# Kernel tuning notes

Hardware: AMD Instinct MI355X
Metric: run time of the kernel (lower is better)

## Reference

```python
import jax, jax.numpy as jnp
import numpy as np

NUM_HEADS = 16
CHUNK = 128


def _bitlinear(x, w, b):
    # BitLinear 1.58b: ternary weights + int8 activations with STE (forward value is exact quantized math)
    w_scale = jnp.maximum(jnp.mean(jnp.abs(w)), 1e-5)
    w_norm = w / w_scale
    w_q = jax.lax.stop_gradient(jnp.sign(w_norm) - w_norm) + w_norm
    x_scale = jnp.maximum(jnp.max(jnp.abs(x), axis=-1, keepdims=True), 1e-5)
    x_norm = x / x_scale * 127.0
    x_q = jax.lax.stop_gradient(jnp.round(x_norm) - x_norm) + x_norm
    return jnp.einsum('...i,oi->...o', x_q, w_q) * (x_scale * w_scale / 127.0) + b


def _rmsnorm(x, w, eps=1e-6):
    return x * jax.lax.rsqrt(jnp.mean(x * x, axis=-1, keepdims=True) + eps) * w


def setup_inputs():
    key = jax.random.key(0)
    ks = jax.random.split(key, 8)
    B, N, C = 2, 4096, 2048
    def w(k, shape):
        return jax.random.normal(k, shape, jnp.float32) * 0.02
    return {
        'x': jax.random.normal(ks[0], (B, N, C), jnp.float32),
        'qkv_w': w(ks[1], (3 * C, C)), 'qkv_b': w(ks[2], (3 * C,)),
        'gate_w': w(ks[3], (C, C)), 'gate_b': w(ks[4], (C,)),
        'proj_w': w(ks[5], (C, C)), 'proj_b': w(ks[6], (C,)),
        'norm_w': jnp.ones((C,), jnp.float32),
    }


def reference(x, qkv_w, qkv_b, gate_w, gate_b, proj_w, proj_b, norm_w):
    B, N, C = x.shape
    H, L = NUM_HEADS, CHUNK
    D = C // H
    scale = D ** -0.5
    qkv = _bitlinear(x, qkv_w, qkv_b).reshape(B, N, 3, H, D)
    q, k, v = qkv[:, :, 0], qkv[:, :, 1], qkv[:, :, 2]
    g = jax.nn.sigmoid(_bitlinear(x, gate_w, gate_b)).reshape(B, N, H, D)
    nc = N // L  # N chosen as multiple of chunk_size -> pad branch is a no-op

    def chunks(t):  # (B,N,H,D) -> (nc,B,L,H,D) for scan over chunks
        return t.reshape(B, nc, L, H, D).transpose(1, 0, 2, 3, 4)
    qc, kc, vc, gc = map(chunks, (q, k, v, g))

    def step(kv_state, inp):
        qi, ki, vi, gi = inp  # each (B,L,H,D)
        # faithful to torch: qi @ ki.transpose(-2,-1) contracts head_dim per position -> (B,L,H,H)
        attn = jax.nn.softmax(jnp.einsum('blhd,blgd->blhg', qi, ki) * scale, axis=-1)
        local = jnp.einsum('blhg,blgd->blhd', attn, vi)
        recur = jnp.einsum('blhd,bhde->blhe', qi, kv_state)
        decay = jnp.mean(gi, axis=1)[..., None]          # (B,H,D,1)
        kv_update = jnp.einsum('blhd,blhe->bhde', ki, vi)
        return kv_state * decay + kv_update, local + recur

    kv0 = jnp.zeros((B, H, D, D), x.dtype)
    _, out = jax.lax.scan(step, kv0, (qc, kc, vc, gc))  # out: (nc,B,L,H,D)
    out = out.transpose(1, 0, 2, 3, 4).reshape(B, N, C)
    return _bitlinear(_rmsnorm(out, norm_w), proj_w, proj_b)
```

## Files before the change

kernel.cpp:

```cpp
#include <hip/hip_runtime.h>
#include <stdint.h>

typedef __attribute__((ext_vector_type(4))) float f32x4;
typedef __attribute__((ext_vector_type(8))) __bf16 bf16x8;
typedef __attribute__((ext_vector_type(4))) unsigned int u32x4;
typedef __attribute__((ext_vector_type(4))) int i32x4;

#define DEV static __device__ __forceinline__

DEV float bf2f(unsigned short h){ union{unsigned int u; float f;} v; v.u=((unsigned int)h)<<16; return v.f; }
DEV unsigned short f2bf(float f){ union{float ff; unsigned int u;} v; v.ff=f; unsigned int u=v.u;
  u += 0x7fffu + ((u>>16)&1u); return (unsigned short)(u>>16); }

DEV f32x4 mfma16(bf16x8 a, bf16x8 b, f32x4 c){
  return __builtin_amdgcn_mfma_f32_16x16x32_bf16(a, b, c, 0, 0, 0);
}
DEV i32x4 mfma_i8(i32x4 a, i32x4 b, i32x4 c){
  return __builtin_amdgcn_mfma_i32_16x16x64_i8(a, b, c, 0, 0, 0);
}

#define GLOAD_LDS16(gptr, ldsptr) \
  __builtin_amdgcn_global_load_lds( \
      (const __attribute__((address_space(1))) unsigned int*)(gptr), \
      (__attribute__((address_space(3))) unsigned int*)(ldsptr), 16, 0, 0)

__global__ __launch_bounds__(256) void k_quant_w(
    const float* __restrict__ wq, const float* __restrict__ wg, const float* __restrict__ wp,
    signed char* __restrict__ oq, signed char* __restrict__ og, signed char* __restrict__ op,
    float* __restrict__ partials)
{
  int blk = blockIdx.x, t = threadIdx.x;
  const float* src; signed char* dst; long base;
  if (blk < 3072){ src=wq; dst=oq; base=(long)blk*4096; }
  else if (blk < 4096){ src=wg; dst=og; base=(long)(blk-3072)*4096; }
  else { src=wp; dst=op; base=(long)(blk-4096)*4096; }
  float s = 0.f;
  #pragma unroll
  for (int i=0;i<4;i++){
    long e = base + (long)(i*256 + t)*4;
    float4 v = *reinterpret_cast<const float4*>(src + e);
    s += fabsf(v.x)+fabsf(v.y)+fabsf(v.z)+fabsf(v.w);
    signed char tmp[4];
    tmp[0] = (v.x>0.f)?1:((v.x<0.f)?-1:0);
    tmp[1] = (v.y>0.f)?1:((v.y<0.f)?-1:0);
    tmp[2] = (v.z>0.f)?1:((v.z<0.f)?-1:0);
    tmp[3] = (v.w>0.f)?1:((v.w<0.f)?-1:0);
    *reinterpret_cast<unsigned int*>(dst + e) = *reinterpret_cast<unsigned int*>(tmp);
  }
  #pragma unroll
  for (int m=1;m<64;m<<=1) s += __shfl_xor(s, m);
  __shared__ float red[4];
  if ((t&63)==0) red[t>>6]=s;
  __syncthreads();
  if (t==0) partials[blk] = red[0]+red[1]+red[2]+red[3];
}

__global__ void k_finalize(const float* __restrict__ partials, float* __restrict__ scales)
{
  int t = threadIdx.x;
  __shared__ float red[4];
  for (int w=0; w<3; w++){
    int s0 = (w==0)?0:((w==1)?3072:4096);
    int s1 = (w==0)?3072:((w==1)?4096:5120);
    float acc = 0.f;
    for (int i=s0+t; i<s1; i+=256) acc += partials[i];
    #pragma unroll
    for (int m=1;m<64;m<<=1) acc += __shfl_xor(acc, m);
    if ((t&63)==0) red[t>>6]=acc;
    __syncthreads();
    if (t==0){
      float total = red[0]+red[1]+red[2]+red[3];
      float denom = (w==0)? 12582912.0f : 4194304.0f;
      float wsc = fmaxf(total/denom, 1e-5f);
      scales[w] = wsc / 127.0f;
    }
    __syncthreads();
  }
}

__global__ __launch_bounds__(256) void k_quant_x(const float* __restrict__ x,
    signed char* __restrict__ xq, float* __restrict__ xs)
{
  int row=blockIdx.x, t=threadIdx.x;
  const float* xr = x + (long)row*2048;
  float v[8];
  float4 a = *reinterpret_cast<const float4*>(xr + t*8);
  float4 b = *reinterpret_cast<const float4*>(xr + t*8 + 4);
  v[0]=a.x; v[1]=a.y; v[2]=a.z; v[3]=a.w; v[4]=b.x; v[5]=b.y; v[6]=b.z; v[7]=b.w;
  float mx=0.f;
  #pragma unroll
  for (int j=0;j<8;j++) mx = fmaxf(mx, fabsf(v[j]));
  #pragma unroll
  for (int m=1;m<64;m<<=1) mx = fmaxf(mx, __shfl_xor(mx, m));
  __shared__ float red[4];
  if ((t&63)==0) red[t>>6]=mx;
  __syncthreads();
  float sc = fmaxf(fmaxf(fmaxf(red[0],red[1]),fmaxf(red[2],red[3])), 1e-5f);
  if (t==0) xs[row]=sc;
  signed char q[8];
  #pragma unroll
  for (int j=0;j<8;j++) q[j] = (signed char)(int)rintf((v[j]/sc)*127.f);
  *reinterpret_cast<uint2*>(xq + (long)row*2048 + t*8) = *reinterpret_cast<uint2*>(q);
}

template<int MODE>
__global__ __launch_bounds__(256) void k_gemm(
    const signed char* __restrict__ A, const signed char* __restrict__ Bw,
    const float* __restrict__ xs, const float* __restrict__ scales, const float* __restrict__ bias,
    unsigned short* __restrict__ oq, unsigned short* __restrict__ ok, unsigned short* __restrict__ ov,
    float* __restrict__ decay, float* __restrict__ of32)
{
  __shared__ signed char As[2][128*128];
  __shared__ signed char Bs[2][128*128];
  const int K = 2048, NT = 16;
  int tid=threadIdx.x;
  int bn=blockIdx.x, bm=blockIdx.y;
  long n0=(long)bn*128, m0=(long)bm*128;
  int wave=tid>>6, lane=tid&63, l15=lane&15, l4=lane>>4;
  int wr=wave>>1, wc=wave&1;
  int srow = wave*8 + (lane>>3);
  int scol = ((lane&7) ^ ((lane>>3)&7))*16;
  i32x4 z4 = {0,0,0,0};
  i32x4 acc[4][4];
  #pragma unroll
  for (int i=0;i<4;i++)
    #pragma unroll
    for (int j=0;j<4;j++) acc[i][j]=z4;

#define STAGE_ALL(buf, kt) do{ \
    GLOAD_LDS16(A  + (m0 +  0 + srow)*K + (kt) + scol, &As[buf][(  0 + wave*8)*128]); \
    GLOAD_LDS16(A  + (m0 + 32 + srow)*K + (kt) + scol, &As[buf][( 32 + wave*8)*128]); \
    GLOAD_LDS16(A  + (m0 + 64 + srow)*K + (kt) + scol, &As[buf][( 64 + wave*8)*128]); \
    GLOAD_LDS16(A  + (m0 + 96 + srow)*K + (kt) + scol, &As[buf][( 96 + wave*8)*128]); \
    GLOAD_LDS16(Bw + (n0 +  0 + srow)*K + (kt) + scol, &Bs[buf][(  0 + wave*8)*128]); \
    GLOAD_LDS16(Bw + (n0 + 32 + srow)*K + (kt) + scol, &Bs[buf][( 32 + wave*8)*128]); \
    GLOAD_LDS16(Bw + (n0 + 64 + srow)*K + (kt) + scol, &Bs[buf][( 64 + wave*8)*128]); \
    GLOAD_LDS16(Bw + (n0 + 96 + srow)*K + (kt) + scol, &Bs[buf][( 96 + wave*8)*128]); }while(0)
#define RD_A(buf, mr, kk) (*reinterpret_cast<const i32x4*>(&As[buf][(wr*64+(mr)*16+l15)*128 + ((((kk)*4+l4) ^ (l15&7))<<4)]))
#define RD_B(buf, nr, kk) (*reinterpret_cast<const i32x4*>(&Bs[buf][(wc*64+(nr)*16+l15)*128 + ((((kk)*4+l4) ^ (l15&7))<<4)]))

  STAGE_ALL(0, 0);

  for (int t=0; t<NT; ++t){
    int c = t&1;
    if (t+1 < NT){
      STAGE_ALL(c^1, (t+1)*128);
      asm volatile("s_waitcnt vmcnt(8)" ::: "memory");
    } else {
      asm volatile("s_waitcnt vmcnt(0)" ::: "memory");
    }
    __builtin_amdgcn_s_barrier();
    __builtin_amdgcn_s_setprio(1);
    #pragma unroll
    for (int kk=0;kk<2;kk++){
      i32x4 af[4], bfr[4];
      #pragma unroll
      for (int mr=0;mr<4;mr++) af[mr] = RD_A(c,mr,kk);
      #pragma unroll
      for (int nr=0;nr<4;nr++) bfr[nr] = RD_B(c,nr,kk);
      #pragma unroll
      for (int mr=0;mr<4;mr++)
        #pragma unroll
        for (int nr=0;nr<4;nr++)
          acc[mr][nr] = mfma_i8(af[mr], bfr[nr], acc[mr][nr]);
    }
    __builtin_amdgcn_s_setprio(0);
    if (t+1 < NT) __builtin_amdgcn_s_barrier();
  }

  float fac = scales[MODE];
  float xsv[4][4];
  #pragma unroll
  for (int mr=0;mr<4;mr++)
    #pragma unroll
    for (int r2=0;r2<4;r2++)
      xsv[mr][r2] = xs[m0 + wr*64 + mr*16 + 4*l4 + r2] * fac;

  if (MODE==0){
    int sidx = (int)(n0 >> 11);
    unsigned short* dst = (sidx==0)?oq:((sidx==1)?ok:ov);
    int c0 = (int)(n0 & 2047);
    #pragma unroll
    for (int nr=0;nr<4;nr++){
      int c = c0 + wc*64 + nr*16 + l15;
      float bv = bias[n0 + wc*64 + nr*16 + l15];
      #pragma unroll
      for (int mr=0;mr<4;mr++)
        #pragma unroll
        for (int r2=0;r2<4;r2++){
          long grow = m0 + wr*64 + mr*16 + 4*l4 + r2;
          dst[grow*2048 + c] = f2bf((float)acc[mr][nr][r2]*xsv[mr][r2] + bv);
        }
    }
  } else if (MODE==1){
    float* red = reinterpret_cast<float*>(As);
    #pragma unroll
    for (int nr=0;nr<4;nr++){
      float bv = bias[n0 + wc*64 + nr*16 + l15];
      float ssum = 0.f;
      #pragma unroll
      for (int mr=0;mr<4;mr++)
        #pragma unroll
        for (int r2=0;r2<4;r2++){
          float val = (float)acc[mr][nr][r2]*xsv[mr][r2] + bv;
          ssum += 1.f/(1.f + expf(-val));
        }
      ssum += __shfl_xor(ssum, 16);
      ssum += __shfl_xor(ssum, 32);
      if (l4==0) red[wr*128 + wc*64 + nr*16 + l15] = ssum;
    }
    __syncthreads();
    if (tid < 128){
      float d = (red[tid] + red[128+tid]) * (1.0f/128.0f);
      decay[((long)bm*16 + bn)*128 + tid] = d;
    }
  } else {
    #pragma unroll
    for (int nr=0;nr<4;nr++){
      long c = n0 + wc*64 + nr*16 + l15;
      float bv = bias[c];
      #pragma unroll
      for (int mr=0;mr<4;mr++)
        #pragma unroll
        for (int r2=0;r2<4;r2++){
          long grow = m0 + wr*64 + mr*16 + 4*l4 + r2;
          of32[grow*2048 + c] = (float)acc[mr][nr][r2]*xsv[mr][r2] + bv;
        }
    }
  }
#undef STAGE_ALL
#undef RD_A
#undef RD_B
}

__global__ __launch_bounds__(256) void k_attnA(const unsigned short* __restrict__ qb,
    const unsigned short* __restrict__ kb, const unsigned short* __restrict__ vb,
    unsigned short* __restrict__ aof)
{
  __shared__ unsigned short at[4][16*32];
  __shared__ unsigned short vT[4][128*40];
  int tid=threadIdx.x, wave=tid>>6, lane=tid&63, l15=lane&15, l4=lane>>4;
  const float SCALE = 0.08838834764831845f;

  for (int i=lane;i<16*32;i+=64) at[wave][i]=0;
  for (int i=lane;i<128*40;i+=64) vT[wave][i]=0;

  long token = (long)blockIdx.x*4 + wave;
  long base = token*2048;

  bf16x8 qf[4], kf[4];
  #pragma unroll
  for (int kk=0;kk<4;kk++){
    qf[kk] = *reinterpret_cast<const bf16x8*>(qb + base + l15*128 + kk*32 + l4*8);
    kf[kk] = *reinterpret_cast<const bf16x8*>(kb + base + l15*128 + kk*32 + l4*8);
  }
  {
    int g = lane>>2, e0 = (lane&3)*32;
    #pragma unroll
    for (int j=0;j<4;j++){
      u32x4 vv = *reinterpret_cast<const u32x4*>(vb + base + g*128 + e0 + j*8);
      unsigned short tmp[8];
      *reinterpret_cast<u32x4*>(tmp) = vv;
      #pragma unroll
      for (int t2=0;t2<8;t2++) vT[wave][(e0+j*8+t2)*40 + g] = tmp[t2];
    }
  }

  f32x4 s = {0.f,0.f,0.f,0.f};
  #pragma unroll
  for (int kk=0;kk<4;kk++) s = mfma16(qf[kk], kf[kk], s);

  #pragma unroll
  for (int r2=0;r2<4;r2++){
    float v = s[r2];
    float m = v;
    m = fmaxf(m, __shfl_xor(m,1)); m = fmaxf(m, __shfl_xor(m,2));
    m = fmaxf(m, __shfl_xor(m,4)); m = fmaxf(m, __shfl_xor(m,8));
    float p = expf((v-m)*SCALE);
    float sum = p;
    sum += __shfl_xor(sum,1); sum += __shfl_xor(sum,2);
    sum += __shfl_xor(sum,4); sum += __shfl_xor(sum,8);
    at[wave][(4*l4+r2)*32 + l15] = f2bf(p/sum);
  }
  __syncthreads();

  bf16x8 pa = *reinterpret_cast<const bf16x8*>(&at[wave][l15*32 + l4*8]);
  #pragma unroll
  for (int eb=0;eb<8;eb++){
    bf16x8 vf = *reinterpret_cast<const bf16x8*>(&vT[wave][(eb*16+l15)*40 + l4*8]);
    f32x4 z4 = {0.f,0.f,0.f,0.f};
    f32x4 o = mfma16(pa, vf, z4);
    #pragma unroll
    for (int r2=0;r2<4;r2++)
      aof[base + (long)(4*l4+r2)*128 + eb*16 + l15] = f2bf(o[r2]);
  }
}

__global__ __launch_bounds__(256) void k_updB1(
    const unsigned short* __restrict__ kb, const unsigned short* __restrict__ vb,
    float* __restrict__ upds)
{
  __shared__ unsigned short kT[128*128];
  __shared__ unsigned short vT[128*128];
  int bid=blockIdx.x;
  int ch = bid&31, h=(bid>>5)&15, b=bid>>9;
  int tid=threadIdx.x, wave=tid>>6, lane=tid&63, l15=lane&15, l4=lane>>4;
  long base = ((long)b*4096 + (long)ch*128)*2048 + h*128;

  #pragma unroll
  for (int i=0;i<8;i++){
    int s = tid + i*256;
    int l = s>>4, sl = s&15;
    unsigned short tmp[8];
    u32x4 v1 = *reinterpret_cast<const u32x4*>(kb + base + (long)l*2048 + sl*8);
    *reinterpret_cast<u32x4*>(tmp) = v1;
    #pragma unroll
    for (int j=0;j<8;j++){
      int d = sl*8+j;
      kT[d*128 + (((l>>3)^(d&15))<<3) + (l&7)] = tmp[j];
    }
    u32x4 v2 = *reinterpret_cast<const u32x4*>(vb + base + (long)l*2048 + sl*8);
    *reinterpret_cast<u32x4*>(tmp) = v2;
    #pragma unroll
    for (int j=0;j<8;j++){
      int e = sl*8+j;
      vT[e*128 + (((l>>3)^(e&15))<<3) + (l&7)] = tmp[j];
    }
  }
  __syncthreads();

  f32x4 z4 = {0.f,0.f,0.f,0.f};
  f32x4 acc[2][8];
  #pragma unroll
  for (int er=0;er<2;er++)
    #pragma unroll
    for (int dc=0;dc<8;dc++) acc[er][dc]=z4;

  #pragma unroll
  for (int kk=0;kk<4;kk++){
    bf16x8 xf[2];
    #pragma unroll
    for (int er=0;er<2;er++){
      int e = wave*32 + er*16 + l15;
      xf[er] = *reinterpret_cast<const bf16x8*>(vT + e*128 + (((kk*4+l4)^(e&15))<<3));
    }
    #pragma unroll
    for (int dc=0;dc<8;dc++){
      int d = dc*16 + l15;
      bf16x8 kf = *reinterpret_cast<const bf16x8*>(kT + d*128 + (((kk*4+l4)^(d&15))<<3));
      #pragma unroll
      for (int er=0;er<2;er++)
        acc[er][dc] = mfma16(xf[er], kf, acc[er][dc]);
    }
  }

  float* dst = upds + (long)bid*16384;
  #pragma unroll
  for (int er=0;er<2;er++)
    #pragma unroll
    for (int dc=0;dc<8;dc++)
      #pragma unroll
      for (int r2=0;r2<4;r2++){
        int e = wave*32 + er*16 + 4*l4 + r2;
        int d = dc*16 + l15;
        dst[e*128 + d] = acc[er][dc][r2];
      }
}

__global__ __launch_bounds__(256) void k_scanB2(float* __restrict__ buf,
    const float* __restrict__ decay)
{
  int bid=blockIdx.x;
  int strip = bid&7, bh = bid>>3;
  int b = bh>>4, h = bh&15;
  int t = threadIdx.x;
  int f0 = t, f1 = t + 256;
  int e0 = strip*16 + (f0>>5), d0 = (f0&31)*4;
  int e1 = strip*16 + (f1>>5);
  long base = (long)bh * 32 * 16384;
  long o0 = (long)e0*128 + d0;
  long o1 = (long)e1*128 + d0;
  float4 s0 = {0.f,0.f,0.f,0.f}, s1 = {0.f,0.f,0.f,0.f};
  for (int ch=0; ch<32; ch++){
    float* p = buf + base + (long)ch*16384;
    float4 u0 = *reinterpret_cast<float4*>(p + o0);
    float4 u1 = *reinterpret_cast<float4*>(p + o1);
    *reinterpret_cast<float4*>(p + o0) = s0;
    *reinterpret_cast<float4*>(p + o1) = s1;
    float4 dc = *reinterpret_cast<const float4*>(decay + ((long)(b*32+ch)*16 + h)*128 + d0);
    s0.x = s0.x*dc.x + u0.x; s0.y = s0.y*dc.y + u0.y;
    s0.z = s0.z*dc.z + u0.z; s0.w = s0.w*dc.w + u0.w;
    s1.x = s1.x*dc.x + u1.x; s1.y = s1.y*dc.y + u1.y;
    s1.z = s1.z*dc.z + u1.z; s1.w = s1.w*dc.w + u1.w;
  }
}

__global__ __launch_bounds__(256) void k_recurB3(
    const unsigned short* __restrict__ qb, const float* __restrict__ upds,
    unsigned short* __restrict__ aof)
{
  __shared__ unsigned short sh[128*128];
  __shared__ unsigned short slo[128*128];
  int bid=blockIdx.x;
  int ch = bid&31, h=(bid>>5)&15, b=bid>>9;
  int tid=threadIdx.x, wave=tid>>6, lane=tid&63, l15=lane&15, l4=lane>>4;
  long slab = (long)bid*16384;
  long base = ((long)b*4096 + (long)ch*128)*2048 + h*128;

  #pragma unroll
  for (int i=0;i<8;i++){
    int s = tid + i*256;
    int e = s>>4, sl = s&15;
    float4 a = *reinterpret_cast<const float4*>(upds + slab + (long)e*128 + sl*8);
    float4 c = *reinterpret_cast<const float4*>(upds + slab + (long)e*128 + sl*8 + 4);
    float vv[8] = {a.x,a.y,a.z,a.w,c.x,c.y,c.z,c.w};
    unsigned short hi[8], lo[8];
    #pragma unroll
    for (int j=0;j<8;j++){
      hi[j] = f2bf(vv[j]);
      lo[j] = f2bf(vv[j] - bf2f(hi[j]));
    }
    int slot = e*128 + ((sl ^ (e&15))<<3);
    *reinterpret_cast<u32x4*>(sh + slot)  = *reinterpret_cast<u32x4*>(hi);
    *reinterpret_cast<u32x4*>(slo + slot) = *reinterpret_cast<u32x4*>(lo);
  }

  bf16x8 qf[2][4];
  #pragma unroll
  for (int mr=0;mr<2;mr++)
    #pragma unroll
    for (int kk=0;kk<4;kk++)
      qf[mr][kk] = *reinterpret_cast<const bf16x8*>(qb + base + (long)(wave*32+mr*16+l15)*2048 + kk*32 + l4*8);
  __syncthreads();

  f32x4 z4 = {0.f,0.f,0.f,0.f};
  f32x4 acc[2][8];
  #pragma unroll
  for (int mr=0;mr<2;mr++)
    #pragma unroll
    for (int ec=0;ec<8;ec++) acc[mr][ec]=z4;

  #pragma unroll
  for (int kk=0;kk<4;kk++)
    #pragma unroll
    for (int ec=0;ec<8;ec++){
      int e = ec*16 + l15;
      int slot = (((kk*4+l4)^(e&15))<<3);
      bf16x8 tfh = *reinterpret_cast<const bf16x8*>(sh + e*128 + slot);
      bf16x8 tfl = *reinterpret_cast<const bf16x8*>(slo + e*128 + slot);
      #pragma unroll
      for (int mr=0;mr<2;mr++){
        acc[mr][ec] = mfma16(qf[mr][kk], tfh, acc[mr][ec]);
        acc[mr][ec] = mfma16(qf[mr][kk], tfl, acc[mr][ec]);
      }
    }

  #pragma unroll
  for (int mr=0;mr<2;mr++)
    #pragma unroll
    for (int ec=0;ec<8;ec++)
      #pragma unroll
      for (int r2=0;r2<4;r2++){
        long o = base + (long)(wave*32+mr*16+4*l4+r2)*2048 + ec*16 + l15;
        aof[o] = f2bf(bf2f(aof[o]) + acc[mr][ec][r2]);
      }
}

__global__ __launch_bounds__(256) void k_rmsnorm_quant(const unsigned short* __restrict__ ain,
    const float* __restrict__ normw, signed char* __restrict__ x2q, float* __restrict__ xs2)
{
  int row=blockIdx.x, t=threadIdx.x;
  const unsigned short* rp = ain + (long)row*2048;
  u32x4 raw = *reinterpret_cast<const u32x4*>(rp + t*8);
  unsigned short tmp[8];
  *reinterpret_cast<u32x4*>(tmp) = raw;
  float xv[8]; float ss=0.f;
  #pragma unroll
  for (int j=0;j<8;j++){ xv[j]=bf2f(tmp[j]); ss += xv[j]*xv[j]; }
  #pragma unroll
  for (int m=1;m<64;m<<=1) ss += __shfl_xor(ss, m);
  __shared__ float red[4];
  if ((t&63)==0) red[t>>6]=ss;
  __syncthreads();
  float ms = (red[0]+red[1]+red[2]+red[3])*(1.0f/2048.0f) + 1e-6f;
  float rs = 1.0f/sqrtf(ms);
  __syncthreads();
  float4 w0 = *reinterpret_cast<const float4*>(normw + t*8);
  float4 w1 = *reinterpret_cast<const float4*>(normw + t*8 + 4);
  float wv[8] = {w0.x,w0.y,w0.z,w0.w,w1.x,w1.y,w1.z,w1.w};
  float y[8]; float mx=0.f;
  #pragma unroll
  for (int j=0;j<8;j++){ y[j] = xv[j]*rs*wv[j]; mx = fmaxf(mx, fabsf(y[j])); }
  #pragma unroll
  for (int m=1;m<64;m<<=1) mx = fmaxf(mx, __shfl_xor(mx, m));
  __shared__ float red2[4];
  if ((t&63)==0) red2[t>>6]=mx;
  __syncthreads();
  float sc = fmaxf(fmaxf(fmaxf(red2[0],red2[1]),fmaxf(red2[2],red2[3])), 1e-5f);
  if (t==0) xs2[row]=sc;
  signed char q[8];
  #pragma unroll
  for (int j=0;j<8;j++) q[j] = (signed char)(int)rintf((y[j]/sc)*127.f);
  *reinterpret_cast<uint2*>(x2q + (long)row*2048 + t*8) = *reinterpret_cast<uint2*>(q);
}

extern "C" void kernel_launch(void* const* d_in, const int* in_sizes, int n_in,
                              void* d_out, int out_size, void* d_ws, size_t ws_size,
                              hipStream_t stream)
{
  const float* x      = (const float*)d_in[0];
  const float* qkv_w  = (const float*)d_in[1];
  const float* qkv_b  = (const float*)d_in[2];
  const float* gate_w = (const float*)d_in[3];
  const float* gate_b = (const float*)d_in[4];
  const float* proj_w = (const float*)d_in[5];
  const float* proj_b = (const float*)d_in[6];
  const float* norm_w = (const float*)d_in[7];
  (void)in_sizes; (void)n_in; (void)out_size; (void)ws_size;

  char* ws = (char*)d_ws;
  const size_t MB = 1024UL*1024UL;
  signed char* wq_proj = (signed char*)(ws + 0*MB);
  signed char* wq_qkv  = (signed char*)(ws + 4*MB);
  signed char* wq_gate = (signed char*)(ws + 16*MB);
  signed char* xq      = (signed char*)(ws + 20*MB);
  float*       upds    = (float*)(ws + 4*MB);
  unsigned short* qb   = (unsigned short*)(ws + 68*MB);
  unsigned short* kb   = (unsigned short*)(ws + 100*MB);
  unsigned short* vb   = (unsigned short*)(ws + 132*MB);
  unsigned short* aof  = (unsigned short*)(ws + 164*MB);
  signed char* x2q     = (signed char*)qb;
  float* xs       = (float*)(ws + 196*MB);
  float* xs2      = xs + 8192;
  float* decay    = xs2 + 8192;
  float* partials = decay + 131072;
  float* scales   = partials + 5120;

  k_quant_w<<<5120,256,0,stream>>>(qkv_w, gate_w, proj_w, wq_qkv, wq_gate, wq_proj, partials);
  k_finalize<<<1,256,0,stream>>>(partials, scales);
  k_quant_x<<<8192,256,0,stream>>>(x, xq, xs);
  k_gemm<0><<<dim3(48,64),256,0,stream>>>(xq, wq_qkv, xs, scales, qkv_b,
      qb,kb,vb, nullptr, nullptr);
  k_gemm<1><<<dim3(16,64),256,0,stream>>>(xq, wq_gate, xs, scales, gate_b,
      nullptr,nullptr,nullptr, decay, nullptr);
  k_attnA<<<2048,256,0,stream>>>(qb,kb,vb, aof);
  k_updB1<<<1024,256,0,stream>>>(kb, vb, upds);
  k_scanB2<<<256,256,0,stream>>>(upds, decay);
  k_recurB3<<<1024,256,0,stream>>>(qb, upds, aof);
  k_rmsnorm_quant<<<8192,256,0,stream>>>(aof, norm_w, x2q, xs2);
  k_gemm<2><<<dim3(16,64),256,0,stream>>>(x2q, wq_proj, xs2, scales, proj_b,
      nullptr,nullptr,nullptr, nullptr, (float*)d_out);
}
```

Baseline: 402.5 us.

## Fuse QKV and gate GEMMs into one launch with XCD-aware tile swizzle

The QKV and gate projection GEMMs now run as a single launch over 64 column tiles. This relies on the gate weights sitting right after the QKV weights in the workspace. Blocks with bn>=48 run the gate/decay epilogue, and the rest write q/k/v. A new 1D block-to-tile mapping spreads consecutive block IDs across the 8 XCDs and groups tiles into 8x8 supertiles, so tiles sharing A and B operands run on the same L2. The aim is to improve cache reuse and cut launch and tail overhead. The cost is that correctness now depends on that workspace layout.

```diff
diff --git a/kernel.cpp b/kernel.cpp
--- a/kernel.cpp
+++ b/kernel.cpp
@@ -103,10 +103,11 @@
   *reinterpret_cast<uint2*>(xq + (long)row*2048 + t*8) = *reinterpret_cast<uint2*>(q);
 }
 
-template<int MODE>
+template<int MODE, int NBN>
 __global__ __launch_bounds__(256) void k_gemm(
     const signed char* __restrict__ A, const signed char* __restrict__ Bw,
-    const float* __restrict__ xs, const float* __restrict__ scales, const float* __restrict__ bias,
+    const float* __restrict__ xs, const float* __restrict__ scales,
+    const float* __restrict__ bias0, const float* __restrict__ bias1,
     unsigned short* __restrict__ oq, unsigned short* __restrict__ ok, unsigned short* __restrict__ ov,
     float* __restrict__ decay, float* __restrict__ of32)
 {
@@ -114,7 +115,11 @@
   __shared__ signed char Bs[2][128*128];
   const int K = 2048, NT = 16;
   int tid=threadIdx.x;
-  int bn=blockIdx.x, bm=blockIdx.y;
+  const int nwg = NBN*64, cpx = nwg>>3;
+  int wg  = ((int)blockIdx.x & 7)*cpx + ((int)blockIdx.x >> 3);
+  int super = wg >> 6, inner = wg & 63;
+  int bn = (super % (NBN>>3))*8 + (inner & 7);
+  int bm = (super / (NBN>>3))*8 + (inner >> 3);
   long n0=(long)bn*128, m0=(long)bm*128;
   int wave=tid>>6, lane=tid&63, l15=lane&15, l4=lane>>4;
   int wr=wave>>1, wc=wave&1;
@@ -168,22 +173,21 @@
     if (t+1 < NT) __builtin_amdgcn_s_barrier();
   }
 
-  float fac = scales[MODE];
-  float xsv[4][4];
-  #pragma unroll
-  for (int mr=0;mr<4;mr++)
-    #pragma unroll
-    for (int r2=0;r2<4;r2++)
-      xsv[mr][r2] = xs[m0 + wr*64 + mr*16 + 4*l4 + r2] * fac;
-
-  if (MODE==0){
+  if (MODE==0 && bn < 48){
+    float fac = scales[0];
+    float xsv[4][4];
+    #pragma unroll
+    for (int mr=0;mr<4;mr++)
+      #pragma unroll
+      for (int r2=0;r2<4;r2++)
+        xsv[mr][r2] = xs[m0 + wr*64 + mr*16 + 4*l4 + r2] * fac;
     int sidx = (int)(n0 >> 11);
     unsigned short* dst = (sidx==0)?oq:((sidx==1)?ok:ov);
     int c0 = (int)(n0 & 2047);
     #pragma unroll
     for (int nr=0;nr<4;nr++){
       int c = c0 + wc*64 + nr*16 + l15;
-      float bv = bias[n0 + wc*64 + nr*16 + l15];
+      float bv = bias0[n0 + wc*64 + nr*16 + l15];
       #pragma unroll
       for (int mr=0;mr<4;mr++)
         #pragma unroll
@@ -192,11 +196,19 @@
           dst[grow*2048 + c] = f2bf((float)acc[mr][nr][r2]*xsv[mr][r2] + bv);
         }
     }
-  } else if (MODE==1){
+  } else if (MODE==0){
+    int bng = bn - 48;
+    float fac = scales[1];
+    float xsv[4][4];
+    #pragma unroll
+    for (int mr=0;mr<4;mr++)
+      #pragma unroll
+      for (int r2=0;r2<4;r2++)
+        xsv[mr][r2] = xs[m0 + wr*64 + mr*16 + 4*l4 + r2] * fac;
     float* red = reinterpret_cast<float*>(As);
     #pragma unroll
     for (int nr=0;nr<4;nr++){
-      float bv = bias[n0 + wc*64 + nr*16 + l15];
+      float bv = bias1[bng*128 + wc*64 + nr*16 + l15];
       float ssum = 0.f;
       #pragma unroll
       for (int mr=0;mr<4;mr++)
@@ -212,13 +224,20 @@
     __syncthreads();
     if (tid < 128){
       float d = (red[tid] + red[128+tid]) * (1.0f/128.0f);
-      decay[((long)bm*16 + bn)*128 + tid] = d;
+      decay[((long)bm*16 + bng)*128 + tid] = d;
     }
   } else {
+    float fac = scales[2];
+    float xsv[4][4];
+    #pragma unroll
+    for (int mr=0;mr<4;mr++)
+      #pragma unroll
+      for (int r2=0;r2<4;r2++)
+        xsv[mr][r2] = xs[m0 + wr*64 + mr*16 + 4*l4 + r2] * fac;
     #pragma unroll
     for (int nr=0;nr<4;nr++){
       long c = n0 + wc*64 + nr*16 + l15;
-      float bv = bias[c];
+      float bv = bias0[c];
       #pragma unroll
       for (int mr=0;mr<4;mr++)
         #pragma unroll
@@ -539,15 +558,13 @@
   k_quant_w<<<5120,256,0,stream>>>(qkv_w, gate_w, proj_w, wq_qkv, wq_gate, wq_proj, partials);
   k_finalize<<<1,256,0,stream>>>(partials, scales);
   k_quant_x<<<8192,256,0,stream>>>(x, xq, xs);
-  k_gemm<0><<<dim3(48,64),256,0,stream>>>(xq, wq_qkv, xs, scales, qkv_b,
-      qb,kb,vb, nullptr, nullptr);
-  k_gemm<1><<<dim3(16,64),256,0,stream>>>(xq, wq_gate, xs, scales, gate_b,
-      nullptr,nullptr,nullptr, decay, nullptr);
+  k_gemm<0,64><<<4096,256,0,stream>>>(xq, wq_qkv, xs, scales, qkv_b, gate_b,
+      qb,kb,vb, decay, nullptr);
   k_attnA<<<2048,256,0,stream>>>(qb,kb,vb, aof);
   k_updB1<<<1024,256,0,stream>>>(kb, vb, upds);
   k_scanB2<<<256,256,0,stream>>>(upds, decay);
   k_recurB3<<<1024,256,0,stream>>>(qb, upds, aof);
   k_rmsnorm_quant<<<8192,256,0,stream>>>(aof, norm_w, x2q, xs2);
-  k_gemm<2><<<dim3(16,64),256,0,stream>>>(x2q, wq_proj, xs2, scales, proj_b,
+  k_gemm<2,16><<<1024,256,0,stream>>>(x2q, wq_proj, xs2, scales, proj_b, nullptr,
       nullptr,nullptr,nullptr, nullptr, (float*)d_out);
 }
```

Result: no change. 395.1 us (-1.8%).
